# Optimization experiments

Measured on AMD Instinct MI355X. Metric: run time of the kernel, lower is better.

Reference implementation:

```python
import jax, jax.numpy as jnp
import numpy as np

M_TOKENS = 8192
K = 4096
N = 11008
BLOCK = 16
N_BLOCKS = K // BLOCK  # 256


def setup_inputs() -> dict:
    key = jax.random.key(0)
    k1, k2, k3, k4 = jax.random.split(key, 4)
    x = jax.random.normal(k1, (M_TOKENS, K), dtype=jnp.float16)
    # block-diagonal input rotations (DuQuant R_in), 16x16 per block
    R_in = jax.random.normal(k2, (N_BLOCKS, BLOCK, BLOCK), dtype=jnp.float16) * jnp.float16(0.25)
    # per-output-row scales (n_groups = 1, effective_group_size = in_features)
    scales = (jax.random.uniform(k3, (N, 1), dtype=jnp.float32) * 0.02 + 0.005).astype(jnp.float16)
    # symmetric uint4 zero point = 8.0
    zeros = jnp.full((N, 1), 8.0, dtype=jnp.float16)
    # input channel permutation (identity arange is a valid permutation)
    perm = jnp.arange(K, dtype=jnp.int32)
    # uint4 quantized weight values in [0, 15], stored unpacked
    qweight = jax.random.randint(k4, (N, K), 0, 16, dtype=jnp.int32)
    return {"x": x, "R_in": R_in, "scales": scales, "zeros": zeros,
            "perm": perm, "qweight": qweight}


def reference(x, R_in, scales, zeros, perm, qweight):
    # --- DuQuant input transform: permutation + block-diagonal rotation ---
    m = x.shape[0]
    xp = x[:, perm]                                   # [M, K]
    xb = xp.reshape(m, N_BLOCKS, BLOCK)               # [M, nb, 16]
    xt = jnp.einsum('mbi,bij->mbj', xb, R_in).reshape(m, K)  # [M, K] fp16
    # --- Dequantize uint4 weights: W = (q - zero) * scale, per output row ---
    Wd = (qweight.astype(jnp.float16) - zeros) * scales        # [N, K] fp16
    # --- W4A16 GEMM with fp32 accumulation, fp16 output ---
    y = jnp.einsum('mk,nk->mn', xt, Wd,
                   preferred_element_type=jnp.float32).astype(jnp.float16)
    return y
```

## Files before the change

kernel.cpp:

```cpp
#include <hip/hip_runtime.h>
#include <hip/hip_bf16.h>
#include <stdint.h>

#define M_TOK 8192
#define KDIM  4096
#define NDIM  11008

typedef float  f32x4  __attribute__((ext_vector_type(4)));
typedef int    i32x4  __attribute__((ext_vector_type(4)));
typedef unsigned short ushort8 __attribute__((ext_vector_type(8)));

__device__ __forceinline__ unsigned short f2b(float f) {
    union { float f; unsigned int i; } v; v.f = f;
    unsigned int u = v.i;
    unsigned int r = (u + 0x7fffu + ((u >> 16) & 1u)) >> 16;
    return (unsigned short)r;
}
__device__ __forceinline__ float b2f(unsigned short u) {
    union { unsigned int i; float f; } v; v.i = ((unsigned int)u) << 16; return v.f;
}

__device__ __forceinline__ void gl_lds16(const void* g, void* l) {
    __builtin_amdgcn_global_load_lds(
        (const __attribute__((address_space(1))) unsigned int*)g,
        (__attribute__((address_space(3))) unsigned int*)l, 16, 0, 0);
}

__global__ __launch_bounds__(256) void prep1_kernel(
    const float* __restrict__ x, const float* __restrict__ R,
    const int* __restrict__ perm, const int* __restrict__ qw,
    unsigned short* __restrict__ xt, float* __restrict__ pmax,
    signed char* __restrict__ q8)
{
    const int bid = blockIdx.x;
    const int t   = threadIdx.x;

    if (bid < 8192) {
        __shared__ float Rs[16 * 273];
        __shared__ int   ps[256];
        const int bg = bid & 15;
        const int mc = bid >> 4;

        ps[t] = perm[bg * 256 + t];
        {
            const float* Rg = R + (size_t)bg * 4096;
#pragma unroll
            for (int k = 0; k < 16; ++k) {
                const int idx = t * 16 + k;
                const int bs = idx >> 8;
                const int i  = (idx >> 4) & 15;
                const int j  = idx & 15;
                Rs[bs * 273 + i * 17 + j] = Rg[idx];
            }
        }
        __syncthreads();

        const int bs = t & 15;
        const int r  = t >> 4;
        const int m  = mc * 16 + r;
        const float* xrow = x + (size_t)m * KDIM;

        const int base = ps[bs * 16];
        bool contig = (base & 3) == 0;
#pragma unroll
        for (int i = 1; i < 16; ++i) contig &= (ps[bs * 16 + i] == base + i);

        float xv[16];
        if (contig) {
            const f32x4* xp = (const f32x4*)(xrow + base);
            const f32x4 a0 = xp[0], a1 = xp[1], a2 = xp[2], a3 = xp[3];
#pragma unroll
            for (int i = 0; i < 4; ++i) {
                xv[i]      = a0[i];
                xv[4 + i]  = a1[i];
                xv[8 + i]  = a2[i];
                xv[12 + i] = a3[i];
            }
        } else {
#pragma unroll
            for (int i = 0; i < 16; ++i) xv[i] = xrow[ps[bs * 16 + i]];
        }

        float o[16];
#pragma unroll
        for (int j = 0; j < 16; ++j) o[j] = 0.f;
#pragma unroll
        for (int i = 0; i < 16; ++i) {
            const float xi = xv[i];
            const float* Rrow = &Rs[bs * 273 + i * 17];
#pragma unroll
            for (int j = 0; j < 16; ++j) o[j] += xi * Rrow[j];
        }

        float lm = 0.f;
#pragma unroll
        for (int j = 0; j < 16; ++j) lm = fmaxf(lm, fabsf(o[j]));
#pragma unroll
        for (int k = 1; k < 16; k <<= 1) lm = fmaxf(lm, __shfl_xor(lm, k, 64));
        if (bs == 0) pmax[(size_t)m * 16 + bg] = lm;

        unsigned short os[16] __attribute__((aligned(16)));
#pragma unroll
        for (int j = 0; j < 16; ++j) os[j] = f2b(o[j]);
        unsigned short* dst = xt + (size_t)m * KDIM + bg * 256 + bs * 16;
        *(ushort8*)dst       = *(ushort8*)os;
        *(ushort8*)(dst + 8) = *(ushort8*)(os + 8);
    } else {
        const size_t base = ((size_t)(bid - 8192) * 256 + t) * 16;
        const int4* qp = (const int4*)(qw + base);
        signed char o[16] __attribute__((aligned(16)));
#pragma unroll
        for (int c = 0; c < 4; ++c) {
            const int4 v = qp[c];
            o[c*4+0] = (signed char)v.x; o[c*4+1] = (signed char)v.y;
            o[c*4+2] = (signed char)v.z; o[c*4+3] = (signed char)v.w;
        }
        *(int4*)(q8 + base) = *(const int4*)o;
    }
}

__global__ __launch_bounds__(256) void pack_kernel(
    const unsigned short* __restrict__ xt, const float* __restrict__ pmax,
    signed char* __restrict__ xt8, int* __restrict__ S, float* __restrict__ sa)
{
    const int m = blockIdx.x;
    const int t = threadIdx.x;

    float am = 1e-20f;
#pragma unroll
    for (int i = 0; i < 16; ++i) am = fmaxf(am, pmax[(size_t)m * 16 + i]);
    const float inv = 127.0f / am;

    const unsigned short* src = xt + (size_t)m * KDIM + t * 16;
    ushort8 u0 = *(const ushort8*)src;
    ushort8 u1 = *(const ushort8*)(src + 8);
    signed char qv[16] __attribute__((aligned(16)));
    int s = 0;
#pragma unroll
    for (int i = 0; i < 8; ++i) {
        int q0 = (int)rintf(b2f(u0[i]) * inv);
        q0 = q0 > 127 ? 127 : (q0 < -127 ? -127 : q0);
        qv[i] = (signed char)q0; s += q0;
        int q1 = (int)rintf(b2f(u1[i]) * inv);
        q1 = q1 > 127 ? 127 : (q1 < -127 ? -127 : q1);
        qv[8 + i] = (signed char)q1; s += q1;
    }
    *(int4*)(xt8 + (size_t)m * KDIM + t * 16) = *(const int4*)qv;

#pragma unroll
    for (int k = 1; k < 64; k <<= 1) s += __shfl_xor(s, k, 64);
    __shared__ int ws[4];
    if ((t & 63) == 0) ws[t >> 6] = s;
    __syncthreads();
    if (t == 0) {
        S[m]  = ws[0] + ws[1] + ws[2] + ws[3];
        sa[m] = am * (1.0f / 127.0f);
    }
}

#define BAR() do { asm volatile("" ::: "memory"); __builtin_amdgcn_s_barrier(); \
                   asm volatile("" ::: "memory"); } while (0)
#define WAITV(n) asm volatile("s_waitcnt vmcnt(" #n ")" ::: "memory")
#define PRIO1 __builtin_amdgcn_s_setprio(1)
#define PRIO0 __builtin_amdgcn_s_setprio(0)

#define ABASE(bb) ((bb)*32768)
#define BBASE(bb) ((bb)*32768 + 16384)

#define STAGE_A(bb, kB) do { \
    gl_lds16(aStageBase + (size_t)(  0)*KDIM + (kB), lds + ABASE(bb) +    0 + wOff); \
    gl_lds16(aStageBase + (size_t)(128)*KDIM + (kB), lds + ABASE(bb) + 8192 + wOff); \
} while (0)
#define STAGE_B(bb, kB) do { \
    gl_lds16(bStageBase + (size_t)(  0)*KDIM + (kB), lds + BBASE(bb) +    0 + wOff); \
    gl_lds16(bStageBase + (size_t)(128)*KDIM + (kB), lds + BBASE(bb) + 8192 + wOff); \
} while (0)

#define PH_READ_A2(bb, mh, dst) do { \
    _Pragma("unroll") \
    for (int mf = 0; mf < 4; ++mf) \
        dst[mf] = *(const i32x4*)(lds + ABASE(bb) + aRdBase + ((mh)*64 + mf*16)*64); \
} while (0)
#define PH_READ_B2(bb, nh, dst) do { \
    _Pragma("unroll") \
    for (int nf = 0; nf < 2; ++nf) \
        dst[nf] = *(const i32x4*)(lds + BBASE(bb) + bRdBase + ((nh)*32 + nf*16)*64); \
} while (0)

#define MFMA8(mh, nh, Aset, Bset) do { \
    _Pragma("unroll") \
    for (int mf = 0; mf < 4; ++mf) \
    _Pragma("unroll") \
    for (int nf = 0; nf < 2; ++nf) \
        acc[(mh)*4+mf][(nh)*2+nf] = __builtin_amdgcn_mfma_i32_16x16x64_i8( \
            Aset[mf], Bset[nf], acc[(mh)*4+mf][(nh)*2+nf], 0, 0, 0); \
} while (0)

#define TILE(bb, kB, MODE) do { \
    PH_READ_A2(bb, 0, aF0); PH_READ_B2(bb, 0, bG0); \
    if ((MODE) <= 1) STAGE_B((bb)^1, (kB) + 64); \
    PH_READ_B2(bb, 1, bG1); \
    PRIO1; MFMA8(0, 0, aF0, bG0); PRIO0; \
    PH_READ_A2(bb, 1, aF1); \
    PRIO1; MFMA8(0, 1, aF0, bG1); PRIO0; \
    BAR(); \
    if ((MODE) == 0) STAGE_A(bb, (kB) + 128); \
    PRIO1; MFMA8(1, 0, aF1, bG0); PRIO0; \
    PRIO1; MFMA8(1, 1, aF1, bG1); PRIO0; \
    if ((MODE) == 0) WAITV(2); \
    if ((MODE) == 1) WAITV(0); \
    BAR(); \
} while (0)

#define TAB(bb) ((bb)*24576)
#define TBB(bb) ((bb)*24576 + 8192)

#define STAGE_TA(bb, kB) \
    gl_lds16(aStageBase + (size_t)(0)*KDIM + (kB), lds + TAB(bb) + wOff)
#define STAGE_TB(bb, kB) do { \
    gl_lds16(bStageBase + (size_t)(  0)*KDIM + (kB), lds + TBB(bb) +    0 + wOff); \
    gl_lds16(bStageBase + (size_t)(128)*KDIM + (kB), lds + TBB(bb) + 8192 + wOff); \
} while (0)

#define PH_READ_TA(bb) do { \
    _Pragma("unroll") \
    for (int mf = 0; mf < 4; ++mf) \
        aF[mf] = *(const i32x4*)(lds + TAB(bb) + aRdBase + (mf*16)*64); \
} while (0)
#define PH_READ_TB(bb, nh, dst) do { \
    _Pragma("unroll") \
    for (int nf = 0; nf < 2; ++nf) \
        dst[nf] = *(const i32x4*)(lds + TBB(bb) + bRdBase + ((nh)*32 + nf*16)*64); \
} while (0)

#define MFMA_T8(nh, Bset) do { \
    _Pragma("unroll") \
    for (int mf = 0; mf < 4; ++mf) \
    _Pragma("unroll") \
    for (int nf = 0; nf < 2; ++nf) \
        acc[mf][(nh)*2+nf] = __builtin_amdgcn_mfma_i32_16x16x64_i8( \
            aF[mf], Bset[nf], acc[mf][(nh)*2+nf], 0, 0, 0); \
} while (0)

#define TTILE(bb, kB, MODE) do { \
    PH_READ_TA(bb); PH_READ_TB(bb, 0, bG0); \
    if ((MODE) <= 1) STAGE_TB((bb)^1, (kB) + 64); \
    PH_READ_TB(bb, 1, bG1); \
    PRIO1; MFMA_T8(0, bG0); PRIO0; \
    BAR(); \
    if ((MODE) == 0) STAGE_TA(bb, (kB) + 128); \
    PRIO1; MFMA_T8(1, bG1); PRIO0; \
    if ((MODE) == 0) WAITV(1); \
    if ((MODE) == 1) WAITV(0); \
    BAR(); \
} while (0)

__global__ __launch_bounds__(512, 2) void gemm_all(
    const signed char* __restrict__ Aq, const signed char* __restrict__ Bq,
    const float* __restrict__ sn, const float* __restrict__ zz,
    const float* __restrict__ sa, const int* __restrict__ S,
    float* __restrict__ C)
{
    __shared__ char lds[65536];

    const int tid  = threadIdx.x;
    const int wave = tid >> 6;
    const int lane = tid & 63;
    const int wr   = wave >> 2;
    const int wc   = wave & 3;
    const int wg   = blockIdx.x;

    const int sRow = tid >> 2;
    const int sCol = (tid & 3) * 16;
    const int wOff = wave * 1024;

    const int lane15 = lane & 15;
    const int kq     = (lane >> 4) * 16;

    if (wg < 1280) {
        const int swz = (wg & 7) * 160 + (wg >> 3);
        const int Sx = swz >> 7;
        const int L  = swz & 127;
        const int tm = L >> 2;
        const int tn = (Sx << 2) + (L & 3);

        const char* aStageBase = (const char*)Aq + (size_t)(tm * 256 + sRow) * KDIM + sCol;
        const char* bStageBase = (const char*)Bq + (size_t)(tn * 256 + sRow) * KDIM + sCol;

        const int aRdBase = wr * 8192 + lane15 * 64 + kq;
        const int bRdBase = wc * 4096 + lane15 * 64 + kq;

        i32x4 acc[8][4] = {};
        i32x4 aF0[4], aF1[4];
        i32x4 bG0[2], bG1[2];

        STAGE_A(0, 0);
        STAGE_B(0, 0);
        STAGE_A(1, 64);
        WAITV(2);
        BAR();

        int kB = 0;
#pragma unroll 1
        for (int t = 0; t < 61; t += 2) {
            TILE(0, kB, 0);
            TILE(1, kB + 64, 0);
            kB += 128;
        }
        TILE(0, 62 * 64, 1);
        TILE(1, 63 * 64, 2);

        const int row0 = tm * 256 + wr * 128 + (lane >> 4) * 4;
        const int col0 = tn * 256 + wc * 64 + lane15;
        float sn4[4], z4[4];
#pragma unroll
        for (int ni = 0; ni < 4; ++ni) { sn4[ni] = sn[col0 + ni*16]; z4[ni] = zz[col0 + ni*16]; }
#pragma unroll
        for (int mi = 0; mi < 8; ++mi) {
            const int rbase = row0 + mi * 16;
            float sa4[4], Sf4[4];
#pragma unroll
            for (int j = 0; j < 4; ++j) { sa4[j] = sa[rbase + j]; Sf4[j] = (float)S[rbase + j]; }
#pragma unroll
            for (int ni = 0; ni < 4; ++ni) {
                const i32x4 v = acc[mi][ni];
                const int c = col0 + ni * 16;
#pragma unroll
                for (int j = 0; j < 4; ++j)
                    C[(size_t)(rbase + j) * NDIM + c] = sa4[j] * sn4[ni] * ((float)v[j] - z4[ni] * Sf4[j]);
            }
        }
    } else {
        const int h   = wg - 1280;
        const int tn  = 40 + (h % 3);
        const int tmh = h / 3;

        const char* aStageBase = (const char*)Aq + (size_t)(tmh * 128 + sRow) * KDIM + sCol;
        const char* bStageBase = (const char*)Bq + (size_t)(tn * 256 + sRow) * KDIM + sCol;

        const int aRdBase = wr * 4096 + lane15 * 64 + kq;
        const int bRdBase = wc * 4096 + lane15 * 64 + kq;

        i32x4 acc[4][4] = {};
        i32x4 aF[4];
        i32x4 bG0[2], bG1[2];

        STAGE_TA(0, 0);
        STAGE_TB(0, 0);
        STAGE_TA(1, 64);
        WAITV(1);
        BAR();

        int kB = 0;
#pragma unroll 1
        for (int t = 0; t < 61; t += 2) {
            TTILE(0, kB, 0);
            TTILE(1, kB + 64, 0);
            kB += 128;
        }
        TTILE(0, 62 * 64, 1);
        TTILE(1, 63 * 64, 2);

        const int row0 = tmh * 128 + wr * 64 + (lane >> 4) * 4;
        const int col0 = tn * 256 + wc * 64 + lane15;
        float sn4[4], z4[4];
#pragma unroll
        for (int ni = 0; ni < 4; ++ni) { sn4[ni] = sn[col0 + ni*16]; z4[ni] = zz[col0 + ni*16]; }
#pragma unroll
        for (int mi = 0; mi < 4; ++mi) {
            const int rbase = row0 + mi * 16;
            float sa4[4], Sf4[4];
#pragma unroll
            for (int j = 0; j < 4; ++j) { sa4[j] = sa[rbase + j]; Sf4[j] = (float)S[rbase + j]; }
#pragma unroll
            for (int ni = 0; ni < 4; ++ni) {
                const i32x4 v = acc[mi][ni];
                const int c = col0 + ni * 16;
#pragma unroll
                for (int j = 0; j < 4; ++j)
                    C[(size_t)(rbase + j) * NDIM + c] = sa4[j] * sn4[ni] * ((float)v[j] - z4[ni] * Sf4[j]);
            }
        }
    }
}

extern "C" void kernel_launch(void* const* d_in, const int* in_sizes, int n_in,
                              void* d_out, int out_size, void* d_ws, size_t ws_size,
                              hipStream_t stream) {
    const float* x      = (const float*)d_in[0];
    const float* R      = (const float*)d_in[1];
    const float* scales = (const float*)d_in[2];
    const float* zeros  = (const float*)d_in[3];
    const int*   perm   = (const int*)d_in[4];
    const int*   qw     = (const int*)d_in[5];
    float*       out    = (float*)d_out;

    char* ws = (char*)d_ws;
    unsigned short* xt16 = (unsigned short*)ws;
    signed char*    xt8  = (signed char*)(ws + 67108864);
    signed char*    q8   = (signed char*)(ws + 100663296);
    float*          pmax = (float*)(ws + 145752064);
    float*          sa   = (float*)(ws + 146276352);
    int*            S    = (int*)(ws + 146309120);

    prep1_kernel<<<dim3(8192 + 11008), 256, 0, stream>>>(x, R, perm, qw, xt16, pmax, q8);
    pack_kernel<<<dim3(M_TOK), 256, 0, stream>>>(xt16, pmax, xt8, S, sa);
    gemm_all<<<dim3(1472), 512, 0, stream>>>(xt8, q8, scales, zeros, sa, S, out);
}
```

Before: 464.2 us.

## Switch int8 GEMM to uniform 128x128 tiles with XOR-swizzled LDS and K=128 steps

Replaces the 256x256-tile main kernel and its 128x256 tail path with a single 128x128 tile per 256-thread workgroup, covering the grid with a grouped swizzle. Each K step grows from 64 to 128 bytes, and the LDS columns are XOR-swizzled on both the global-to-LDS stores and the fragment reads to avoid bank conflicts. This removes the divergent tail path and gives more workgroups for balance, at the cost of lower arithmetic intensity per tile and more global traffic for A and B.

```diff
diff --git a/kernel.cpp b/kernel.cpp
--- a/kernel.cpp
+++ b/kernel.cpp
@@ -168,94 +168,55 @@
 #define BBASE(bb) ((bb)*32768 + 16384)
 
 #define STAGE_A(bb, kB) do { \
-    gl_lds16(aStageBase + (size_t)(  0)*KDIM + (kB), lds + ABASE(bb) +    0 + wOff); \
-    gl_lds16(aStageBase + (size_t)(128)*KDIM + (kB), lds + ABASE(bb) + 8192 + wOff); \
+    gl_lds16(aStageBase + (size_t)( 0)*KDIM + (kB), lds + ABASE(bb) +     0 + wOff); \
+    gl_lds16(aStageBase + (size_t)(32)*KDIM + (kB), lds + ABASE(bb) +  4096 + wOff); \
+    gl_lds16(aStageBase + (size_t)(64)*KDIM + (kB), lds + ABASE(bb) +  8192 + wOff); \
+    gl_lds16(aStageBase + (size_t)(96)*KDIM + (kB), lds + ABASE(bb) + 12288 + wOff); \
 } while (0)
 #define STAGE_B(bb, kB) do { \
-    gl_lds16(bStageBase + (size_t)(  0)*KDIM + (kB), lds + BBASE(bb) +    0 + wOff); \
-    gl_lds16(bStageBase + (size_t)(128)*KDIM + (kB), lds + BBASE(bb) + 8192 + wOff); \
-} while (0)
-
-#define PH_READ_A2(bb, mh, dst) do { \
+    gl_lds16(bStageBase + (size_t)( 0)*KDIM + (kB), lds + BBASE(bb) +     0 + wOff); \
+    gl_lds16(bStageBase + (size_t)(32)*KDIM + (kB), lds + BBASE(bb) +  4096 + wOff); \
+    gl_lds16(bStageBase + (size_t)(64)*KDIM + (kB), lds + BBASE(bb) +  8192 + wOff); \
+    gl_lds16(bStageBase + (size_t)(96)*KDIM + (kB), lds + BBASE(bb) + 12288 + wOff); \
+} while (0)
+
+#define PH_READ_A(bb) do { \
     _Pragma("unroll") \
-    for (int mf = 0; mf < 4; ++mf) \
-        dst[mf] = *(const i32x4*)(lds + ABASE(bb) + aRdBase + ((mh)*64 + mf*16)*64); \
-} while (0)
-#define PH_READ_B2(bb, nh, dst) do { \
+    for (int mf = 0; mf < 4; ++mf) { \
+        aF[mf][0] = *(const i32x4*)(lds + ABASE(bb) + aRdBase + (mf*16)*128 + cs0); \
+        aF[mf][1] = *(const i32x4*)(lds + ABASE(bb) + aRdBase + (mf*16)*128 + cs1); \
+    } \
+} while (0)
+#define PH_READ_B(bb) do { \
     _Pragma("unroll") \
-    for (int nf = 0; nf < 2; ++nf) \
-        dst[nf] = *(const i32x4*)(lds + BBASE(bb) + bRdBase + ((nh)*32 + nf*16)*64); \
-} while (0)
-
-#define MFMA8(mh, nh, Aset, Bset) do { \
+    for (int nf = 0; nf < 4; ++nf) { \
+        bF[nf][0] = *(const i32x4*)(lds + BBASE(bb) + bRdBase + (nf*16)*128 + cs0); \
+        bF[nf][1] = *(const i32x4*)(lds + BBASE(bb) + bRdBase + (nf*16)*128 + cs1); \
+    } \
+} while (0)
+
+#define MFMA_H(h) do { \
     _Pragma("unroll") \
     for (int mf = 0; mf < 4; ++mf) \
     _Pragma("unroll") \
-    for (int nf = 0; nf < 2; ++nf) \
-        acc[(mh)*4+mf][(nh)*2+nf] = __builtin_amdgcn_mfma_i32_16x16x64_i8( \
-            Aset[mf], Bset[nf], acc[(mh)*4+mf][(nh)*2+nf], 0, 0, 0); \
+    for (int nf = 0; nf < 4; ++nf) \
+        acc[mf][nf] = __builtin_amdgcn_mfma_i32_16x16x64_i8( \
+            aF[mf][h], bF[nf][h], acc[mf][nf], 0, 0, 0); \
 } while (0)
 
 #define TILE(bb, kB, MODE) do { \
-    PH_READ_A2(bb, 0, aF0); PH_READ_B2(bb, 0, bG0); \
-    if ((MODE) <= 1) STAGE_B((bb)^1, (kB) + 64); \
-    PH_READ_B2(bb, 1, bG1); \
-    PRIO1; MFMA8(0, 0, aF0, bG0); PRIO0; \
-    PH_READ_A2(bb, 1, aF1); \
-    PRIO1; MFMA8(0, 1, aF0, bG1); PRIO0; \
+    PH_READ_A(bb); PH_READ_B(bb); \
+    if ((MODE) <= 1) STAGE_B((bb)^1, (kB) + 128); \
+    PRIO1; MFMA_H(0); PRIO0; \
     BAR(); \
-    if ((MODE) == 0) STAGE_A(bb, (kB) + 128); \
-    PRIO1; MFMA8(1, 0, aF1, bG0); PRIO0; \
-    PRIO1; MFMA8(1, 1, aF1, bG1); PRIO0; \
-    if ((MODE) == 0) WAITV(2); \
+    if ((MODE) == 0) STAGE_A(bb, (kB) + 256); \
+    PRIO1; MFMA_H(1); PRIO0; \
+    if ((MODE) == 0) WAITV(4); \
     if ((MODE) == 1) WAITV(0); \
     BAR(); \
 } while (0)
 
-#define TAB(bb) ((bb)*24576)
-#define TBB(bb) ((bb)*24576 + 8192)
-
-#define STAGE_TA(bb, kB) \
-    gl_lds16(aStageBase + (size_t)(0)*KDIM + (kB), lds + TAB(bb) + wOff)
-#define STAGE_TB(bb, kB) do { \
-    gl_lds16(bStageBase + (size_t)(  0)*KDIM + (kB), lds + TBB(bb) +    0 + wOff); \
-    gl_lds16(bStageBase + (size_t)(128)*KDIM + (kB), lds + TBB(bb) + 8192 + wOff); \
-} while (0)
-
-#define PH_READ_TA(bb) do { \
-    _Pragma("unroll") \
-    for (int mf = 0; mf < 4; ++mf) \
-        aF[mf] = *(const i32x4*)(lds + TAB(bb) + aRdBase + (mf*16)*64); \
-} while (0)
-#define PH_READ_TB(bb, nh, dst) do { \
-    _Pragma("unroll") \
-    for (int nf = 0; nf < 2; ++nf) \
-        dst[nf] = *(const i32x4*)(lds + TBB(bb) + bRdBase + ((nh)*32 + nf*16)*64); \
-} while (0)
-
-#define MFMA_T8(nh, Bset) do { \
-    _Pragma("unroll") \
-    for (int mf = 0; mf < 4; ++mf) \
-    _Pragma("unroll") \
-    for (int nf = 0; nf < 2; ++nf) \
-        acc[mf][(nh)*2+nf] = __builtin_amdgcn_mfma_i32_16x16x64_i8( \
-            aF[mf], Bset[nf], acc[mf][(nh)*2+nf], 0, 0, 0); \
-} while (0)
-
-#define TTILE(bb, kB, MODE) do { \
-    PH_READ_TA(bb); PH_READ_TB(bb, 0, bG0); \
-    if ((MODE) <= 1) STAGE_TB((bb)^1, (kB) + 64); \
-    PH_READ_TB(bb, 1, bG1); \
-    PRIO1; MFMA_T8(0, bG0); PRIO0; \
-    BAR(); \
-    if ((MODE) == 0) STAGE_TA(bb, (kB) + 128); \
-    PRIO1; MFMA_T8(1, bG1); PRIO0; \
-    if ((MODE) == 0) WAITV(1); \
-    if ((MODE) == 1) WAITV(0); \
-    BAR(); \
-} while (0)
-
-__global__ __launch_bounds__(512, 2) void gemm_all(
+__global__ __launch_bounds__(256, 2) void gemm_all(
     const signed char* __restrict__ Aq, const signed char* __restrict__ Bq,
     const float* __restrict__ sn, const float* __restrict__ zz,
     const float* __restrict__ sa, const int* __restrict__ S,
@@ -266,120 +227,75 @@
     const int tid  = threadIdx.x;
     const int wave = tid >> 6;
     const int lane = tid & 63;
-    const int wr   = wave >> 2;
-    const int wc   = wave & 3;
+    const int wr   = wave >> 1;
+    const int wc   = wave & 1;
     const int wg   = blockIdx.x;
 
-    const int sRow = tid >> 2;
-    const int sCol = (tid & 3) * 16;
+    const int swz = (wg & 7) * 688 + (wg >> 3);
+    int tm, tn;
+    if (swz < 5120) {
+        const int Sx = swz >> 9;
+        const int L  = swz & 511;
+        tm = L >> 3;
+        tn = (Sx << 3) + (L & 7);
+    } else {
+        const int L = swz - 5120;
+        tm = L / 6;
+        tn = 80 + (L - tm * 6);
+    }
+
+    const int sRow    = tid >> 3;
+    const int gColSwz = (((tid & 7) ^ (sRow & 7)) << 4);
+    const char* aStageBase = (const char*)Aq + (size_t)(tm * 128 + sRow) * KDIM + gColSwz;
+    const char* bStageBase = (const char*)Bq + (size_t)(tn * 128 + sRow) * KDIM + gColSwz;
     const int wOff = wave * 1024;
 
     const int lane15 = lane & 15;
-    const int kq     = (lane >> 4) * 16;
-
-    if (wg < 1280) {
-        const int swz = (wg & 7) * 160 + (wg >> 3);
-        const int Sx = swz >> 7;
-        const int L  = swz & 127;
-        const int tm = L >> 2;
-        const int tn = (Sx << 2) + (L & 3);
-
-        const char* aStageBase = (const char*)Aq + (size_t)(tm * 256 + sRow) * KDIM + sCol;
-        const char* bStageBase = (const char*)Bq + (size_t)(tn * 256 + sRow) * KDIM + sCol;
-
-        const int aRdBase = wr * 8192 + lane15 * 64 + kq;
-        const int bRdBase = wc * 4096 + lane15 * 64 + kq;
-
-        i32x4 acc[8][4] = {};
-        i32x4 aF0[4], aF1[4];
-        i32x4 bG0[2], bG1[2];
-
-        STAGE_A(0, 0);
-        STAGE_B(0, 0);
-        STAGE_A(1, 64);
-        WAITV(2);
-        BAR();
-
-        int kB = 0;
+    const int lx  = (lane & 7) << 4;
+    const int kq  = (lane >> 4) * 16;
+    const int cs0 = kq ^ lx;
+    const int cs1 = (kq + 64) ^ lx;
+    const int aRdBase = wr * 8192 + lane15 * 128;
+    const int bRdBase = wc * 8192 + lane15 * 128;
+
+    i32x4 acc[4][4] = {};
+    i32x4 aF[4][2];
+    i32x4 bF[4][2];
+
+    STAGE_A(0, 0);
+    STAGE_B(0, 0);
+    STAGE_A(1, 128);
+    WAITV(4);
+    BAR();
+
+    int kB = 0;
 #pragma unroll 1
-        for (int t = 0; t < 61; t += 2) {
-            TILE(0, kB, 0);
-            TILE(1, kB + 64, 0);
-            kB += 128;
-        }
-        TILE(0, 62 * 64, 1);
-        TILE(1, 63 * 64, 2);
-
-        const int row0 = tm * 256 + wr * 128 + (lane >> 4) * 4;
-        const int col0 = tn * 256 + wc * 64 + lane15;
-        float sn4[4], z4[4];
-#pragma unroll
-        for (int ni = 0; ni < 4; ++ni) { sn4[ni] = sn[col0 + ni*16]; z4[ni] = zz[col0 + ni*16]; }
-#pragma unroll
-        for (int mi = 0; mi < 8; ++mi) {
-            const int rbase = row0 + mi * 16;
-            float sa4[4], Sf4[4];
-#pragma unroll
-            for (int j = 0; j < 4; ++j) { sa4[j] = sa[rbase + j]; Sf4[j] = (float)S[rbase + j]; }
-#pragma unroll
-            for (int ni = 0; ni < 4; ++ni) {
-                const i32x4 v = acc[mi][ni];
-                const int c = col0 + ni * 16;
-#pragma unroll
-                for (int j = 0; j < 4; ++j)
-                    C[(size_t)(rbase + j) * NDIM + c] = sa4[j] * sn4[ni] * ((float)v[j] - z4[ni] * Sf4[j]);
-            }
-        }
-    } else {
-        const int h   = wg - 1280;
-        const int tn  = 40 + (h % 3);
-        const int tmh = h / 3;
-
-        const char* aStageBase = (const char*)Aq + (size_t)(tmh * 128 + sRow) * KDIM + sCol;
-        const char* bStageBase = (const char*)Bq + (size_t)(tn * 256 + sRow) * KDIM + sCol;
-
-        const int aRdBase = wr * 4096 + lane15 * 64 + kq;
-        const int bRdBase = wc * 4096 + lane15 * 64 + kq;
-
-        i32x4 acc[4][4] = {};
-        i32x4 aF[4];
-        i32x4 bG0[2], bG1[2];
-
-        STAGE_TA(0, 0);
-        STAGE_TB(0, 0);
-        STAGE_TA(1, 64);
-        WAITV(1);
-        BAR();
-
-        int kB = 0;
-#pragma unroll 1
-        for (int t = 0; t < 61; t += 2) {
-            TTILE(0, kB, 0);
-            TTILE(1, kB + 64, 0);
-            kB += 128;
-        }
-        TTILE(0, 62 * 64, 1);
-        TTILE(1, 63 * 64, 2);
-
-        const int row0 = tmh * 128 + wr * 64 + (lane >> 4) * 4;
-        const int col0 = tn * 256 + wc * 64 + lane15;
-        float sn4[4], z4[4];
-#pragma unroll
-        for (int ni = 0; ni < 4; ++ni) { sn4[ni] = sn[col0 + ni*16]; z4[ni] = zz[col0 + ni*16]; }
-#pragma unroll
-        for (int mi = 0; mi < 4; ++mi) {
-            const int rbase = row0 + mi * 16;
-            float sa4[4], Sf4[4];
-#pragma unroll
-            for (int j = 0; j < 4; ++j) { sa4[j] = sa[rbase + j]; Sf4[j] = (float)S[rbase + j]; }
-#pragma unroll
-            for (int ni = 0; ni < 4; ++ni) {
-                const i32x4 v = acc[mi][ni];
-                const int c = col0 + ni * 16;
-#pragma unroll
-                for (int j = 0; j < 4; ++j)
-                    C[(size_t)(rbase + j) * NDIM + c] = sa4[j] * sn4[ni] * ((float)v[j] - z4[ni] * Sf4[j]);
-            }
+    for (int t = 0; t < 29; t += 2) {
+        TILE(0, kB, 0);
+        TILE(1, kB + 128, 0);
+        kB += 256;
+    }
+    TILE(0, 30 * 128, 1);
+    TILE(1, 31 * 128, 2);
+
+    const int row0 = tm * 128 + wr * 64 + (lane >> 4) * 4;
+    const int col0 = tn * 128 + wc * 64 + lane15;
+    float sn4[4], z4[4];
+#pragma unroll
+    for (int ni = 0; ni < 4; ++ni) { sn4[ni] = sn[col0 + ni*16]; z4[ni] = zz[col0 + ni*16]; }
+#pragma unroll
+    for (int mi = 0; mi < 4; ++mi) {
+        const int rbase = row0 + mi * 16;
+        float sa4[4], Sf4[4];
+#pragma unroll
+        for (int j = 0; j < 4; ++j) { sa4[j] = sa[rbase + j]; Sf4[j] = (float)S[rbase + j]; }
+#pragma unroll
+        for (int ni = 0; ni < 4; ++ni) {
+            const i32x4 v = acc[mi][ni];
+            const int c = col0 + ni * 16;
+#pragma unroll
+            for (int j = 0; j < 4; ++j)
+                C[(size_t)(rbase + j) * NDIM + c] = sa4[j] * sn4[ni] * ((float)v[j] - z4[ni] * Sf4[j]);
         }
     }
 }
@@ -405,5 +321,5 @@
 
     prep1_kernel<<<dim3(8192 + 11008), 256, 0, stream>>>(x, R, perm, qw, xt16, pmax, q8);
     pack_kernel<<<dim3(M_TOK), 256, 0, stream>>>(xt16, pmax, xt8, S, sa);
-    gemm_all<<<dim3(1472), 512, 0, stream>>>(xt8, q8, scales, zeros, sa, S, out);
-}
+    gemm_all<<<dim3((M_TOK / 128) * (NDIM / 128)), 256, 0, stream>>>(xt8, q8, scales, zeros, sa, S, out);
+}
```

After: 458.2 us. Within noise of the previous version (-1.3%).
